# Performance work log

Hardware: AMD Instinct MI355X
Metric: run time of the kernel (lower is better)

Reference implementation:

```python
import jax, jax.numpy as jnp
import numpy as np

B, N, T, H = 64, 16, 128, 256  # batch, max_neighbors, time_steps, hidden_dim


def setup_inputs() -> dict:
    key = jax.random.key(0)
    ks = jax.random.split(key, 7)
    inv_h = 1.0 / np.sqrt(H)
    return {
        "node_rnn_output": jax.random.normal(ks[0], (B, T, H), jnp.float32),
        "neigh_rnn_output": jax.random.normal(ks[1], (B, N, T, H), jnp.float32),
        "neighbors_number": N,
        "Wq": jax.random.normal(ks[2], (H, H), jnp.float32) * inv_h,
        "Wk": jax.random.normal(ks[3], (H, H), jnp.float32) * inv_h,
        "Wv": jax.random.normal(ks[4], (H, H), jnp.float32) * inv_h,
        "Wb": jax.random.normal(ks[5], (H, H), jnp.float32) * inv_h,
        "b": jnp.zeros((T,), jnp.float32),
    }


def reference(node_rnn_output, neigh_rnn_output, neighbors_number, Wq, Wk, Wv, Wb, b):
    # key_values: node prepended to neighbors -> [B, N+1, T, H]
    kv = jnp.concatenate((node_rnn_output[:, None], neigh_rnn_output), axis=1)
    # torch nn.Linear: x @ W^T
    q = node_rnn_output @ Wq.T            # [B, T, H] (query is identical across neighbor slots)
    key = kv @ Wk.T                       # [B, N+1, T, H]
    value = kv @ Wv.T                     # [B, N+1, T, H]
    # bilinear score: (q @ Wb) @ key^T + b  (b broadcasts over last axis)
    qW = q @ Wb                           # [B, T, H]
    S = jnp.einsum('bth,bnsh->bnts', qW, key) + b  # [B, N+1, T, T]
    A = jax.nn.softmax(S, axis=-1)        # dropout is identity at eval / drop_prob=0
    outputs = jnp.einsum('bnts,bnsh->bnth', A, value)  # [B, N+1, T, H]
    return outputs, A
```

## Files before the change

kernel.cpp:

```cpp
#include <hip/hip_runtime.h>
#include <cstdio>


typedef __bf16 bf16;
typedef __attribute__((ext_vector_type(8))) __bf16 bf16x8;
typedef __attribute__((ext_vector_type(4))) __bf16 bf16x4;
typedef __attribute__((ext_vector_type(4))) float floatx4;

#define MFMA_BF16 __builtin_amdgcn_mfma_f32_16x16x32_bf16

__device__ __forceinline__ const float* kv_row_ptr(const float* node, const float* neigh, int bn, int s) {
  int b = bn / 17, nn = bn % 17;
  return (nn == 0) ? node + ((size_t)b * 128 + s) * 256
                   : neigh + (((size_t)b * 16 + (nn - 1)) * 128 + s) * 256;
}

__global__ __launch_bounds__(256) void k_wc(const float* __restrict__ Wq, const float* __restrict__ Wb,
                                            float* __restrict__ Wc) {
  int m = blockIdx.x, h = threadIdx.x;
  float acc = 0.f;
  for (int k = 0; k < 256; ++k) acc = fmaf(Wq[k * 256 + m], Wb[k * 256 + h], acc);
  Wc[m * 256 + h] = acc;
}

__global__ __launch_bounds__(256) void k_we(const float* __restrict__ Wc, const float* __restrict__ Wk,
                                            float* __restrict__ We) {
  int m = blockIdx.x, g = threadIdx.x;
  float acc = 0.f;
  for (int k = 0; k < 256; ++k) acc = fmaf(Wc[m * 256 + k], Wk[k * 256 + g], acc);
  We[m * 256 + g] = acc;
}

__global__ __launch_bounds__(256) void k_wvb(const float* __restrict__ Wv, bf16* __restrict__ Wvb) {
  int i = (blockIdx.x * 256 + threadIdx.x) * 4;
  float4 v = *(const float4*)(Wv + i);
  bf16x4 o;
  o[0] = (bf16)v.x; o[1] = (bf16)v.y; o[2] = (bf16)v.z; o[3] = (bf16)v.w;
  *(bf16x4*)(Wvb + i) = o;
}

__global__ __launch_bounds__(256) void k_qwk(const float* __restrict__ X, const float* __restrict__ W,
                                             float* __restrict__ Y) {
  __shared__ float As[32][64];
  __shared__ float Bs[32][64];
  int tid = threadIdx.x;
  int m0 = blockIdx.x * 64, n0 = blockIdx.y * 64;
  int tx = tid & 15, ty = tid >> 4;
  float acc[4][4] = {};
  int r = tid >> 3, c4 = (tid & 7) * 4;
  int kr = tid >> 4, c4b = (tid & 15) * 4;
  for (int k0 = 0; k0 < 256; k0 += 32) {
#pragma unroll
    for (int p = 0; p < 2; ++p) {
      float4 v = *(const float4*)(X + (size_t)(m0 + r + p * 32) * 256 + k0 + c4);
      As[c4 + 0][r + p * 32] = v.x; As[c4 + 1][r + p * 32] = v.y;
      As[c4 + 2][r + p * 32] = v.z; As[c4 + 3][r + p * 32] = v.w;
    }
#pragma unroll
    for (int p = 0; p < 2; ++p) {
      float4 v = *(const float4*)(W + (size_t)(k0 + kr + p * 16) * 256 + n0 + c4b);
      *(float4*)&Bs[kr + p * 16][c4b] = v;
    }
    __syncthreads();
#pragma unroll 8
    for (int k = 0; k < 32; ++k) {
      float a[4], bb[4];
#pragma unroll
      for (int i = 0; i < 4; ++i) a[i] = As[k][ty * 4 + i];
#pragma unroll
      for (int j = 0; j < 4; ++j) bb[j] = Bs[k][tx * 4 + j];
#pragma unroll
      for (int i = 0; i < 4; ++i)
#pragma unroll
        for (int j = 0; j < 4; ++j) acc[i][j] = fmaf(a[i], bb[j], acc[i][j]);
    }
    __syncthreads();
  }
#pragma unroll
  for (int i = 0; i < 4; ++i) {
    float4 v = make_float4(acc[i][0], acc[i][1], acc[i][2], acc[i][3]);
    *(float4*)(Y + (size_t)(m0 + ty * 4 + i) * 256 + n0 + tx * 4) = v;
  }
}

#define QKS 40
#define ABS 136
#define KVS 68
__global__ __launch_bounds__(256) void k_fused(const float* __restrict__ qWk, const float* __restrict__ node,
                                               const float* __restrict__ neigh, const float* __restrict__ bvec,
                                               const bf16* __restrict__ Wvb,
                                               float* __restrict__ Aout, float* __restrict__ Out) {
  __shared__ __align__(16) char smem[52224];
  bf16* Qhi = (bf16*)smem;
  bf16* Qlo = (bf16*)(smem + 10240);
  bf16* Khi = (bf16*)(smem + 20480);
  bf16* Klo = (bf16*)(smem + 30720);
  bf16* Ab  = (bf16*)smem;
  bf16* Kvb = (bf16*)(smem + 34816);
  bf16* Vt  = (bf16*)(smem + 34816);

  int tid = threadIdx.x;
  int w = tid >> 6, lane = tid & 63, lrow = lane & 15, quad = lane >> 4;
  int bn = blockIdx.x;
  const float* Q = qWk + (size_t)(bn / 17) * 128 * 256;
  const float* K = kv_row_ptr(node, neigh, bn, 0);

  int srow = tid >> 1;
  int skb = (tid & 1) * 16;

  floatx4 acc[2][8];
#pragma unroll
  for (int rt = 0; rt < 2; ++rt)
#pragma unroll
    for (int ct = 0; ct < 8; ++ct) acc[rt][ct] = (floatx4)0.0f;

  for (int k0 = 0; k0 < 256; k0 += 32) {
#pragma unroll
    for (int half = 0; half < 2; ++half) {
      const float* qp = Q + (size_t)srow * 256 + k0 + skb + half * 8;
      const float* kp = K + (size_t)srow * 256 + k0 + skb + half * 8;
      float4 q0 = *(const float4*)qp, q1 = *(const float4*)(qp + 4);
      float4 kk0 = *(const float4*)kp, kk1 = *(const float4*)(kp + 4);
      float qf[8] = {q0.x, q0.y, q0.z, q0.w, q1.x, q1.y, q1.z, q1.w};
      float kf[8] = {kk0.x, kk0.y, kk0.z, kk0.w, kk1.x, kk1.y, kk1.z, kk1.w};
      bf16x8 qh, ql, kh, kl;
#pragma unroll
      for (int u = 0; u < 8; ++u) {
        bf16 h = (bf16)qf[u]; qh[u] = h; ql[u] = (bf16)(qf[u] - (float)h);
        bf16 h2 = (bf16)kf[u]; kh[u] = h2; kl[u] = (bf16)(kf[u] - (float)h2);
      }
      int off = srow * QKS + skb + half * 8;
      *(bf16x8*)&Qhi[off] = qh; *(bf16x8*)&Qlo[off] = ql;
      *(bf16x8*)&Khi[off] = kh; *(bf16x8*)&Klo[off] = kl;
    }
    __syncthreads();
    bf16x8 ah[2], al[2];
#pragma unroll
    for (int rt = 0; rt < 2; ++rt) {
      int off = (w * 32 + rt * 16 + lrow) * QKS + quad * 8;
      ah[rt] = *(const bf16x8*)&Qhi[off];
      al[rt] = *(const bf16x8*)&Qlo[off];
    }
#pragma unroll
    for (int ct = 0; ct < 8; ++ct) {
      int off = (ct * 16 + lrow) * QKS + quad * 8;
      bf16x8 bh = *(const bf16x8*)&Khi[off];
      bf16x8 bl = *(const bf16x8*)&Klo[off];
#pragma unroll
      for (int rt = 0; rt < 2; ++rt) {
        acc[rt][ct] = MFMA_BF16(ah[rt], bh, acc[rt][ct], 0, 0, 0);
        acc[rt][ct] = MFMA_BF16(al[rt], bh, acc[rt][ct], 0, 0, 0);
        acc[rt][ct] = MFMA_BF16(ah[rt], bl, acc[rt][ct], 0, 0, 0);
      }
    }
    __syncthreads();
  }

  float bvv[8];
#pragma unroll
  for (int ct = 0; ct < 8; ++ct) bvv[ct] = bvec[ct * 16 + lrow];
#pragma unroll
  for (int rt = 0; rt < 2; ++rt)
#pragma unroll
    for (int r = 0; r < 4; ++r) {
      float mx = -3.402823466e+38f;
#pragma unroll
      for (int ct = 0; ct < 8; ++ct) {
        float v = acc[rt][ct][r] + bvv[ct];
        acc[rt][ct][r] = v;
        mx = fmaxf(mx, v);
      }
#pragma unroll
      for (int off = 1; off < 16; off <<= 1) mx = fmaxf(mx, __shfl_xor(mx, off, 64));
      float s = 0.f;
#pragma unroll
      for (int ct = 0; ct < 8; ++ct) {
        float e = __expf(acc[rt][ct][r] - mx);
        acc[rt][ct][r] = e;
        s += e;
      }
#pragma unroll
      for (int off = 1; off < 16; off <<= 1) s += __shfl_xor(s, off, 64);
      float inv = 1.f / s;
#pragma unroll
      for (int ct = 0; ct < 8; ++ct) acc[rt][ct][r] *= inv;
    }

  float* Ag = Aout + (size_t)bn * 128 * 128;
#pragma unroll
  for (int rt = 0; rt < 2; ++rt)
#pragma unroll
    for (int r = 0; r < 4; ++r) {
      int row = w * 32 + rt * 16 + quad * 4 + r;
#pragma unroll
      for (int ct = 0; ct < 8; ++ct) {
        int s = ct * 16 + lrow;
        float v = acc[rt][ct][r];
        Ag[(size_t)row * 128 + s] = v;
        Ab[row * ABS + s] = (bf16)v;
      }
    }

  float* Ob = Out + (size_t)bn * 128 * 256;
  int vrow = tid >> 1, vkb = (tid & 1) * 32;
  for (int h0 = 0; h0 < 256; h0 += 64) {
    floatx4 vacc[2][4];
#pragma unroll
    for (int rt = 0; rt < 2; ++rt)
#pragma unroll
      for (int ct = 0; ct < 4; ++ct) vacc[rt][ct] = (floatx4)0.0f;

    for (int k0 = 0; k0 < 256; k0 += 64) {
      bf16x8 bwv[2][4];
#pragma unroll
      for (int ks = 0; ks < 2; ++ks)
#pragma unroll
        for (int ct = 0; ct < 4; ++ct)
          bwv[ks][ct] = *(const bf16x8*)&Wvb[(size_t)(h0 + ct * 16 + lrow) * 256 + k0 + ks * 32 + quad * 8];
      {
        const float* kp = K + (size_t)vrow * 256 + k0 + vkb;
        bf16* d = &Kvb[vrow * KVS + vkb];
#pragma unroll
        for (int j = 0; j < 4; ++j) {
          float4 a = *(const float4*)(kp + j * 8);
          float4 b2 = *(const float4*)(kp + j * 8 + 4);
          bf16x8 o;
          o[0] = (bf16)a.x;  o[1] = (bf16)a.y;  o[2] = (bf16)a.z;  o[3] = (bf16)a.w;
          o[4] = (bf16)b2.x; o[5] = (bf16)b2.y; o[6] = (bf16)b2.z; o[7] = (bf16)b2.w;
          *(bf16x8*)(d + j * 8) = o;
        }
      }
      __syncthreads();
#pragma unroll
      for (int ks = 0; ks < 2; ++ks) {
        bf16x8 af[2];
#pragma unroll
        for (int rt = 0; rt < 2; ++rt)
          af[rt] = *(const bf16x8*)&Kvb[(w * 32 + rt * 16 + lrow) * KVS + ks * 32 + quad * 8];
#pragma unroll
        for (int ct = 0; ct < 4; ++ct)
#pragma unroll
          for (int rt = 0; rt < 2; ++rt)
            vacc[rt][ct] = MFMA_BF16(af[rt], bwv[ks][ct], vacc[rt][ct], 0, 0, 0);
      }
      __syncthreads();
    }

#pragma unroll
    for (int ct = 0; ct < 4; ++ct)
#pragma unroll
      for (int rt = 0; rt < 2; ++rt)
#pragma unroll
        for (int r = 0; r < 4; ++r)
          Vt[(ct * 16 + lrow) * ABS + w * 32 + rt * 16 + quad * 4 + r] = (bf16)vacc[rt][ct][r];
    __syncthreads();

    floatx4 pacc[2][4];
#pragma unroll
    for (int rt = 0; rt < 2; ++rt)
#pragma unroll
      for (int ct = 0; ct < 4; ++ct) pacc[rt][ct] = (floatx4)0.0f;
#pragma unroll
    for (int s0 = 0; s0 < 128; s0 += 32) {
      bf16x8 af[2];
#pragma unroll
      for (int rt = 0; rt < 2; ++rt)
        af[rt] = *(const bf16x8*)&Ab[(w * 32 + rt * 16 + lrow) * ABS + s0 + quad * 8];
#pragma unroll
      for (int ct = 0; ct < 4; ++ct) {
        bf16x8 bv8 = *(const bf16x8*)&Vt[(ct * 16 + lrow) * ABS + s0 + quad * 8];
#pragma unroll
        for (int rt = 0; rt < 2; ++rt)
          pacc[rt][ct] = MFMA_BF16(af[rt], bv8, pacc[rt][ct], 0, 0, 0);
      }
    }
#pragma unroll
    for (int rt = 0; rt < 2; ++rt)
#pragma unroll
      for (int ct = 0; ct < 4; ++ct)
#pragma unroll
        for (int r = 0; r < 4; ++r) {
          int row = w * 32 + rt * 16 + quad * 4 + r;
          Ob[(size_t)row * 256 + h0 + ct * 16 + lrow] = pacc[rt][ct][r];
        }
    __syncthreads();
  }
}

extern "C" void kernel_launch(void* const* d_in, const int* in_sizes, int n_in,
                              void* d_out, int out_size, void* d_ws, size_t ws_size,
                              hipStream_t stream) {
  const float* node  = (const float*)d_in[0];
  const float* neigh = (const float*)d_in[1];
  const float* Wq = (const float*)d_in[3];
  const float* Wk = (const float*)d_in[4];
  const float* Wv = (const float*)d_in[5];
  const float* Wb = (const float*)d_in[6];
  const float* bv = (const float*)d_in[7];

  float* out  = (float*)d_out;
  float* Aout = out + (size_t)64 * 17 * 128 * 256;

  size_t need = (size_t)(65536 + 65536 + 2097152) * 4 + (size_t)65536 * 2;
  if (ws_size < need) { fprintf(stderr, "ws too small: %zu < %zu\n", ws_size, need); return; }
  float* wsf = (float*)d_ws;
  float* Wc  = wsf;
  float* We  = wsf + 65536;
  float* qWk = wsf + 131072;
  bf16*  Wvb = (bf16*)(wsf + 131072 + 2097152);

  k_wvb<<<64, 256, 0, stream>>>(Wv, Wvb);
  k_wc<<<256, 256, 0, stream>>>(Wq, Wb, Wc);
  k_we<<<256, 256, 0, stream>>>(Wc, Wk, We);
  k_qwk<<<dim3(128, 4), 256, 0, stream>>>(node, We, qWk);
  k_fused<<<1088, 256, 0, stream>>>(qWk, node, neigh, bv, Wvb, Aout, out);
}
```

Before: 548.9 us.

## Prefetch Q/K tiles in registers and restructure V projection to skip LDS staging

New measurement: 788.3 us. 43.6% more time.

```diff
diff --git a/kernel.cpp b/kernel.cpp
--- a/kernel.cpp
+++ b/kernel.cpp
@@ -85,7 +85,6 @@
 
 #define QKS 40
 #define ABS 136
-#define KVS 68
 __global__ __launch_bounds__(256) void k_fused(const float* __restrict__ qWk, const float* __restrict__ node,
                                                const float* __restrict__ neigh, const float* __restrict__ bvec,
                                                const bf16* __restrict__ Wvb,
@@ -96,7 +95,6 @@
   bf16* Khi = (bf16*)(smem + 20480);
   bf16* Klo = (bf16*)(smem + 30720);
   bf16* Ab  = (bf16*)smem;
-  bf16* Kvb = (bf16*)(smem + 34816);
   bf16* Vt  = (bf16*)(smem + 34816);
 
   int tid = threadIdx.x;
@@ -114,15 +112,19 @@
 #pragma unroll
     for (int ct = 0; ct < 8; ++ct) acc[rt][ct] = (floatx4)0.0f;
 
+  const float* qb = Q + (size_t)srow * 256 + skb;
+  const float* kb = K + (size_t)srow * 256 + skb;
+  float4 pq[4], pk[4];
+#pragma unroll
+  for (int j = 0; j < 4; ++j) { pq[j] = *(const float4*)(qb + j * 4); pk[j] = *(const float4*)(kb + j * 4); }
+
   for (int k0 = 0; k0 < 256; k0 += 32) {
 #pragma unroll
     for (int half = 0; half < 2; ++half) {
-      const float* qp = Q + (size_t)srow * 256 + k0 + skb + half * 8;
-      const float* kp = K + (size_t)srow * 256 + k0 + skb + half * 8;
-      float4 q0 = *(const float4*)qp, q1 = *(const float4*)(qp + 4);
-      float4 kk0 = *(const float4*)kp, kk1 = *(const float4*)(kp + 4);
-      float qf[8] = {q0.x, q0.y, q0.z, q0.w, q1.x, q1.y, q1.z, q1.w};
-      float kf[8] = {kk0.x, kk0.y, kk0.z, kk0.w, kk1.x, kk1.y, kk1.z, kk1.w};
+      float qf[8] = {pq[half * 2].x, pq[half * 2].y, pq[half * 2].z, pq[half * 2].w,
+                     pq[half * 2 + 1].x, pq[half * 2 + 1].y, pq[half * 2 + 1].z, pq[half * 2 + 1].w};
+      float kf[8] = {pk[half * 2].x, pk[half * 2].y, pk[half * 2].z, pk[half * 2].w,
+                     pk[half * 2 + 1].x, pk[half * 2 + 1].y, pk[half * 2 + 1].z, pk[half * 2 + 1].w};
       bf16x8 qh, ql, kh, kl;
 #pragma unroll
       for (int u = 0; u < 8; ++u) {
@@ -132,6 +134,13 @@
       int off = srow * QKS + skb + half * 8;
       *(bf16x8*)&Qhi[off] = qh; *(bf16x8*)&Qlo[off] = ql;
       *(bf16x8*)&Khi[off] = kh; *(bf16x8*)&Klo[off] = kl;
+    }
+    if (k0 < 224) {
+#pragma unroll
+      for (int j = 0; j < 4; ++j) {
+        pq[j] = *(const float4*)(qb + k0 + 32 + j * 4);
+        pk[j] = *(const float4*)(kb + k0 + 32 + j * 4);
+      }
     }
     __syncthreads();
     bf16x8 ah[2], al[2];
@@ -202,88 +211,76 @@
     }
 
   float* Ob = Out + (size_t)bn * 128 * 256;
-  int vrow = tid >> 1, vkb = (tid & 1) * 32;
-  for (int h0 = 0; h0 < 256; h0 += 64) {
-    floatx4 vacc[2][4];
+  for (int hh = 0; hh < 2; ++hh) {
+    int H0 = hh * 128;
+    floatx4 vacc[2][8];
 #pragma unroll
     for (int rt = 0; rt < 2; ++rt)
 #pragma unroll
-      for (int ct = 0; ct < 4; ++ct) vacc[rt][ct] = (floatx4)0.0f;
-
-    for (int k0 = 0; k0 < 256; k0 += 64) {
-      bf16x8 bwv[2][4];
-#pragma unroll
-      for (int ks = 0; ks < 2; ++ks)
+      for (int ct = 0; ct < 8; ++ct) vacc[rt][ct] = (floatx4)0.0f;
+
+#pragma unroll 2
+    for (int kk = 0; kk < 8; ++kk) {
+      bf16x8 af[2];
+#pragma unroll
+      for (int rt = 0; rt < 2; ++rt) {
+        const float* kp = K + (size_t)(w * 32 + rt * 16 + lrow) * 256 + kk * 32 + quad * 8;
+        float4 a = *(const float4*)kp, b2 = *(const float4*)(kp + 4);
+        bf16x8 o;
+        o[0] = (bf16)a.x;  o[1] = (bf16)a.y;  o[2] = (bf16)a.z;  o[3] = (bf16)a.w;
+        o[4] = (bf16)b2.x; o[5] = (bf16)b2.y; o[6] = (bf16)b2.z; o[7] = (bf16)b2.w;
+        af[rt] = o;
+      }
+#pragma unroll 4
+      for (int ct = 0; ct < 8; ++ct) {
+        bf16x8 bwv = *(const bf16x8*)&Wvb[(size_t)(H0 + ct * 16 + lrow) * 256 + kk * 32 + quad * 8];
+#pragma unroll
+        for (int rt = 0; rt < 2; ++rt)
+          vacc[rt][ct] = MFMA_BF16(af[rt], bwv, vacc[rt][ct], 0, 0, 0);
+      }
+    }
+
+    for (int hc = 0; hc < 2; ++hc) {
+#pragma unroll
+      for (int ct = 0; ct < 4; ++ct)
+#pragma unroll
+        for (int rt = 0; rt < 2; ++rt) {
+          bf16x4 o;
+#pragma unroll
+          for (int r = 0; r < 4; ++r) o[r] = (bf16)vacc[rt][hc * 4 + ct][r];
+          *(bf16x4*)&Vt[(ct * 16 + lrow) * ABS + w * 32 + rt * 16 + quad * 4] = o;
+        }
+      __syncthreads();
+      floatx4 pacc[2][4];
+#pragma unroll
+      for (int rt = 0; rt < 2; ++rt)
+#pragma unroll
+        for (int ct = 0; ct < 4; ++ct) pacc[rt][ct] = (floatx4)0.0f;
+#pragma unroll
+      for (int s0 = 0; s0 < 128; s0 += 32) {
+        bf16x8 paf[2];
+#pragma unroll
+        for (int rt = 0; rt < 2; ++rt)
+          paf[rt] = *(const bf16x8*)&Ab[(w * 32 + rt * 16 + lrow) * ABS + s0 + quad * 8];
+#pragma unroll
+        for (int ct = 0; ct < 4; ++ct) {
+          bf16x8 bv8 = *(const bf16x8*)&Vt[(ct * 16 + lrow) * ABS + s0 + quad * 8];
+#pragma unroll
+          for (int rt = 0; rt < 2; ++rt)
+            pacc[rt][ct] = MFMA_BF16(paf[rt], bv8, pacc[rt][ct], 0, 0, 0);
+        }
+      }
+#pragma unroll
+      for (int rt = 0; rt < 2; ++rt)
 #pragma unroll
         for (int ct = 0; ct < 4; ++ct)
-          bwv[ks][ct] = *(const bf16x8*)&Wvb[(size_t)(h0 + ct * 16 + lrow) * 256 + k0 + ks * 32 + quad * 8];
-      {
-        const float* kp = K + (size_t)vrow * 256 + k0 + vkb;
-        bf16* d = &Kvb[vrow * KVS + vkb];
-#pragma unroll
-        for (int j = 0; j < 4; ++j) {
-          float4 a = *(const float4*)(kp + j * 8);
-          float4 b2 = *(const float4*)(kp + j * 8 + 4);
-          bf16x8 o;
-          o[0] = (bf16)a.x;  o[1] = (bf16)a.y;  o[2] = (bf16)a.z;  o[3] = (bf16)a.w;
-          o[4] = (bf16)b2.x; o[5] = (bf16)b2.y; o[6] = (bf16)b2.z; o[7] = (bf16)b2.w;
-          *(bf16x8*)(d + j * 8) = o;
-        }
-      }
+#pragma unroll
+          for (int r = 0; r < 4; ++r) {
+            int row = w * 32 + rt * 16 + quad * 4 + r;
+            Ob[(size_t)row * 256 + H0 + hc * 64 + ct * 16 + lrow] = pacc[rt][ct][r];
+          }
       __syncthreads();
-#pragma unroll
-      for (int ks = 0; ks < 2; ++ks) {
-        bf16x8 af[2];
-#pragma unroll
-        for (int rt = 0; rt < 2; ++rt)
-          af[rt] = *(const bf16x8*)&Kvb[(w * 32 + rt * 16 + lrow) * KVS + ks * 32 + quad * 8];
-#pragma unroll
-        for (int ct = 0; ct < 4; ++ct)
-#pragma unroll
-          for (int rt = 0; rt < 2; ++rt)
-            vacc[rt][ct] = MFMA_BF16(af[rt], bwv[ks][ct], vacc[rt][ct], 0, 0, 0);
-      }
-      __syncthreads();
-    }
-
-#pragma unroll
-    for (int ct = 0; ct < 4; ++ct)
-#pragma unroll
-      for (int rt = 0; rt < 2; ++rt)
-#pragma unroll
-        for (int r = 0; r < 4; ++r)
-          Vt[(ct * 16 + lrow) * ABS + w * 32 + rt * 16 + quad * 4 + r] = (bf16)vacc[rt][ct][r];
-    __syncthreads();
-
-    floatx4 pacc[2][4];
-#pragma unroll
-    for (int rt = 0; rt < 2; ++rt)
-#pragma unroll
-      for (int ct = 0; ct < 4; ++ct) pacc[rt][ct] = (floatx4)0.0f;
-#pragma unroll
-    for (int s0 = 0; s0 < 128; s0 += 32) {
-      bf16x8 af[2];
-#pragma unroll
-      for (int rt = 0; rt < 2; ++rt)
-        af[rt] = *(const bf16x8*)&Ab[(w * 32 + rt * 16 + lrow) * ABS + s0 + quad * 8];
-#pragma unroll
-      for (int ct = 0; ct < 4; ++ct) {
-        bf16x8 bv8 = *(const bf16x8*)&Vt[(ct * 16 + lrow) * ABS + s0 + quad * 8];
-#pragma unroll
-        for (int rt = 0; rt < 2; ++rt)
-          pacc[rt][ct] = MFMA_BF16(af[rt], bv8, pacc[rt][ct], 0, 0, 0);
-      }
-    }
-#pragma unroll
-    for (int rt = 0; rt < 2; ++rt)
-#pragma unroll
-      for (int ct = 0; ct < 4; ++ct)
-#pragma unroll
-        for (int r = 0; r < 4; ++r) {
-          int row = w * 32 + rt * 16 + quad * 4 + r;
-          Ob[(size_t)row * 256 + h0 + ct * 16 + lrow] = pacc[rt][ct][r];
-        }
-    __syncthreads();
+    }
   }
 }
 
```
